# Optimization experiments

Hardware: AMD Instinct MI355X
Metric: run time of the kernel (lower is better)

## Reference

```python
import jax, jax.numpy as jnp
import numpy as np

VOCAB_BLOCK = 2048
TEMP = 1.0
EPS_LO = 0.2
EPS_HI = 0.3


def setup_inputs() -> dict:
    key = jax.random.key(0)
    k = jax.random.split(key, 6)
    B, S, D, V = 4, 1024, 2048, 32768
    hidden_states = jax.random.normal(k[0], (B, S, D), dtype=jnp.float32)
    # 0.02 init scale keeps logits O(1) so exp/logsumexp stay well-conditioned
    lm_head_kernel = jax.random.normal(k[1], (D, V), dtype=jnp.float32) * 0.02
    input_ids = jax.random.randint(k[2], (B, S), 0, V, dtype=jnp.int32)
    labels = jax.random.randint(k[3], (B, S), 0, 2, dtype=jnp.int32)
    advantages = jax.random.normal(k[4], (B,), dtype=jnp.float32)
    old_per_token_logps = jax.random.normal(k[5], (B, S - 1), dtype=jnp.float32) * 0.1
    return {
        "hidden_states": hidden_states,
        "lm_head_kernel": lm_head_kernel,
        "input_ids": input_ids,
        "labels": labels,
        "advantages": advantages,
        "old_per_token_logps": old_per_token_logps,
    }


def _fused_logps(h, kernel):
    """Streaming logsumexp over vocab blocks; never materializes [B,T,V]."""
    B, T, D = h.shape
    V = kernel.shape[1]
    nb = V // VOCAB_BLOCK
    Wb = kernel.reshape(D, nb, VOCAB_BLOCK).transpose(1, 0, 2)  # [nb, D, bs]

    def step(carry, wb):
        m, s = carry
        lg = jnp.einsum("btd,dv->btv", h, wb) / TEMP  # [B,T,bs]
        bm = lg.max(axis=-1)
        nm = jnp.maximum(m, bm)
        s = s * jnp.exp(m - nm) + jnp.exp(lg - nm[..., None]).sum(axis=-1)
        return (nm, s), None

    init = (jnp.full((B, T), -jnp.inf, dtype=h.dtype), jnp.zeros((B, T), dtype=h.dtype))
    (m, s), _ = jax.lax.scan(step, init, Wb)
    return m + jnp.log(s)  # logsumexp over full vocab, [B,T]


def reference(hidden_states, lm_head_kernel, input_ids, labels, advantages, old_per_token_logps):
    h = hidden_states[:, :-1, :]            # [B,T,D], T = S-1
    chosen = input_ids[:, 1:]               # [B,T]
    mask = labels[:, 1:].astype(jnp.float32)

    # chosen-token logit: gather kernel columns, no full logits tensor
    w_sel = lm_head_kernel.T[chosen]        # [B,T,D]
    chosen_logit = jnp.einsum("btd,btd->bt", h, w_sel) / TEMP

    lse = _fused_logps(h, lm_head_kernel)
    per_token_logps = chosen_logit - lse    # [B,T]

    ratio = jnp.exp(per_token_logps - old_per_token_logps)
    adv = advantages[:, None]
    loss1 = ratio * adv
    loss2 = jnp.clip(ratio, 1.0 - EPS_LO, 1.0 + EPS_HI) * adv
    per_token_loss = -jnp.minimum(loss1, loss2)

    total_valid = mask.sum()
    loss = (per_token_loss * mask).sum() / total_valid
    return loss, jax.lax.stop_gradient(per_token_logps)
```

## Files before the change

### kernel.cpp

```cpp
#include <hip/hip_runtime.h>
#include <hip/hip_bf16.h>

typedef unsigned short u16;
typedef unsigned char u8;
typedef unsigned long long u64;
typedef __attribute__((ext_vector_type(4))) int i32x4;
typedef __attribute__((ext_vector_type(8))) int i32x8;
typedef __attribute__((ext_vector_type(4))) float f32x4;

#define NROWS 4092
#define NROWS_PAD 4096
#define DDIM 2048
#define VDIM 32768
#define NCHUNK 512
#define SC8 0x7F7F7F7F
#define BUFB 65536u

__device__ __forceinline__ u8 f2fp8(float f) {
  union { float f; unsigned u; } v; v.f = f;
  unsigned s = (v.u >> 24) & 0x80u;
  unsigned a = v.u & 0x7FFFFFFFu;
  if (a >= 0x43E80000u) return (u8)(s | 0x7E);
  int e = (int)(a >> 23) - 127;
  unsigned m = a & 0x7FFFFFu;
  if (e < -6) {
    unsigned full = m | 0x800000u;
    int sh = 20 + (-6 - e);
    if (sh > 31) return (u8)s;
    unsigned q = full >> sh;
    unsigned rem = full & ((1u << sh) - 1u), half = 1u << (sh - 1);
    q += (rem > half || (rem == half && (q & 1u)));
    return (u8)(s | q);
  }
  unsigned q = m >> 20, rem = m & 0xFFFFFu;
  q += (rem > 0x80000u || (rem == 0x80000u && (q & 1u)));
  unsigned bits = (((unsigned)(e + 7)) << 3) + q;
  if (bits >= 0x7Fu) bits = 0x7Eu;
  return (u8)(s | bits);
}

__device__ __forceinline__ void gload16(const void* g, void* l) {
  using gp_t = const __attribute__((address_space(1))) unsigned*;
  using lp_t = __attribute__((address_space(3))) unsigned*;
  __builtin_amdgcn_global_load_lds((gp_t)g, (lp_t)(unsigned)(unsigned long long)l,
                                   16, 0, 0);
}

#define BAR() __builtin_amdgcn_s_barrier()
#define SB()  __builtin_amdgcn_sched_barrier(0)
#define SHUF(a, b) __builtin_shufflevector(a, b, 0, 1, 2, 3, 4, 5, 6, 7)

__global__ void init_k(const int* __restrict__ ids, int* __restrict__ chosen,
                       float* __restrict__ chlog, float* __restrict__ accum) {
  int i = blockIdx.x * 256 + threadIdx.x;
  if (i < NROWS_PAD) {
    int v = -1;
    if (i < NROWS) { int b = i / 1023, t = i % 1023; v = ids[b * 1024 + t + 1]; }
    chosen[i] = v;
    chlog[i] = 0.f;
  }
  if (i < 2) accum[i] = 0.f;
}

__global__ void bucket_k(const int* __restrict__ chosen,
                         int* __restrict__ boff, int* __restrict__ bent) {
  __shared__ int cnt[512];
  __shared__ int base[512];
  int tid = threadIdx.x;
  cnt[tid] = 0;
  __syncthreads();
  int loc[8], tile[8];
#pragma unroll
  for (int j = 0; j < 8; ++j) {
    int r = tid + (j << 9);
    int c = chosen[r];
    int ti = (c < 0) ? 512 : (c >> 6);
    tile[j] = ti;
    loc[j] = (ti < 512) ? atomicAdd(&cnt[ti], 1) : 0;
  }
  __syncthreads();
  if (tid == 0) {
    int s = 0;
    for (int i = 0; i < 512; ++i) { base[i] = s; s += cnt[i]; }
  }
  __syncthreads();
  boff[tid] = base[tid];
  if (tid == 511) boff[512] = base[511] + cnt[511];
#pragma unroll
  for (int j = 0; j < 8; ++j) {
    int r = tid + (j << 9);
    if (tile[j] < 512) bent[base[tile[j]] + loc[j]] = (r << 6) | (chosen[r] & 63);
  }
}

__global__ void conv_h(const float* __restrict__ hs, u8* __restrict__ h8) {
  int idx = blockIdx.x * 256 + threadIdx.x;
  int row = idx >> 8;
  int c8 = (idx & 255) << 3;
  u64 o = 0;
  if (row < NROWS) {
    int b = row / 1023, t = row % 1023;
    const float* p = hs + (size_t)((b << 10) + t) * DDIM + c8;
    float4 x = *(const float4*)p, y = *(const float4*)(p + 4);
    o = (u64)f2fp8(x.x * 16.f)        | ((u64)f2fp8(x.y * 16.f) << 8) |
        ((u64)f2fp8(x.z * 16.f) << 16) | ((u64)f2fp8(x.w * 16.f) << 24) |
        ((u64)f2fp8(y.x * 16.f) << 32) | ((u64)f2fp8(y.y * 16.f) << 40) |
        ((u64)f2fp8(y.z * 16.f) << 48) | ((u64)f2fp8(y.w * 16.f) << 56);
  }
  *(u64*)(h8 + (size_t)row * DDIM + c8) = o;
}

__global__ void transpose_w(const float* __restrict__ W, u8* __restrict__ WT8,
                            const float* __restrict__ hs,
                            const int* __restrict__ boff,
                            const int* __restrict__ bent,
                            float* __restrict__ chlog) {
  __shared__ float t32[64][65];
  __shared__ u8 t8[64][68];
  int v0 = blockIdx.x << 6, d0 = blockIdx.y << 6;
  int tid = threadIdx.x;
  int vi = (tid & 15) << 2, dl = tid >> 4;
#pragma unroll
  for (int i = 0; i < 4; ++i) {
    int d = dl + (i << 4);
    float4 w = *(const float4*)(W + (size_t)(d0 + d) * VDIM + v0 + vi);
    t32[d][vi + 0] = w.x; t32[d][vi + 1] = w.y;
    t32[d][vi + 2] = w.z; t32[d][vi + 3] = w.w;
    t8[d][vi + 0] = f2fp8(w.x * 64.f); t8[d][vi + 1] = f2fp8(w.y * 64.f);
    t8[d][vi + 2] = f2fp8(w.z * 64.f); t8[d][vi + 3] = f2fp8(w.w * 64.f);
  }
  __syncthreads();
  int vr = tid >> 2, dc = (tid & 3) << 4;
  union { u8 b[16]; ulonglong2 q; } u;
#pragma unroll
  for (int k = 0; k < 16; ++k) u.b[k] = t8[dc + k][vr];
  *(ulonglong2*)(WT8 + (size_t)(v0 + vr) * DDIM + d0 + dc) = u.q;
  int m0 = boff[blockIdx.x], m1 = boff[blockIdx.x + 1];
  int lane = tid & 63, wv = tid >> 6;
  for (int m = m0 + wv; m < m1; m += 4) {
    int e = bent[m];
    int r = e >> 6, cv = e & 63;
    int b = r / 1023, tt = r % 1023;
    float s = hs[(size_t)((b << 10) + tt) * DDIM + d0 + lane] * t32[lane][cv];
#pragma unroll
    for (int o = 1; o < 64; o <<= 1) s += __shfl_xor(s, o, 64);
    if (lane == 0) atomicAdd(chlog + r, s);
  }
}

__global__ __launch_bounds__(256, 1) void gemm_lse(
    const u8* __restrict__ A, const u8* __restrict__ Bt,
    float2* __restrict__ partials) {
  extern __shared__ u16 smem[];
  char* lds = (char*)smem;

  const int tid = threadIdx.x;
  const int l = tid & 63;
  const int wid = tid >> 6;
  const int wmr = wid >> 1, wnr = wid & 1;
  const int ln = l & 15;
  const int g4 = l >> 4;
  const int xr = ln & 7;

  int bid = blockIdx.x;
  int id = ((bid & 7) << 8) | (bid >> 3);
  int bm = id & 15;
  int bn = id >> 4;
  const int m0 = bm << 8, n0 = bn << 8;

  const u8* Ab = A + (size_t)m0 * DDIM;
  const u8* Bb = Bt + (size_t)n0 * DDIM;

  const unsigned aA0 = (unsigned)((wmr << 14) + (ln << 7)) + (((0 | g4) ^ xr) << 4);
  const unsigned aA1 = (unsigned)((wmr << 14) + (ln << 7)) + (((4 | g4) ^ xr) << 4);
  const unsigned aB0 = 32768u + (unsigned)((wnr << 14) + (ln << 7)) + (((0 | g4) ^ xr) << 4);
  const unsigned aB1 = 32768u + (unsigned)((wnr << 14) + (ln << 7)) + (((4 | g4) ^ xr) << 4);

  const int srow = l >> 3;
  const unsigned selb = (unsigned)(((l & 7) ^ srow) << 4);
  unsigned voff[8];
#pragma unroll
  for (int j = 0; j < 8; ++j)
    voff[j] = (unsigned)(((((j << 2) + wid) << 3) | srow) * 2048) + selb;

#define RFL(x) __builtin_amdgcn_readfirstlane((int)(x))
#define GLL(src, dst) gload16((src), lds + RFL(dst))
#define LD4(off) (*(const i32x4*)(lds + (off)))
#define FRAG(b0, b1, o) SHUF(LD4((b0) + (o)), LD4((b1) + (o)))
#define DSTA(j) (unsigned)((((j) << 2) + wid) << 10)
#define DSTB(j) (32768u + (unsigned)((((j) << 2) + wid) << 10))

  f32x4 acc[8][8] = {};

#pragma unroll
  for (int j = 0; j < 8; ++j) GLL(Ab + voff[j], DSTA(j));
#pragma unroll
  for (int j = 0; j < 8; ++j) GLL(Bb + voff[j], DSTB(j));
  asm volatile("s_waitcnt vmcnt(0)" ::: "memory"); SB();
  BAR();
  SB();

  for (int t = 0; t < 16; ++t) {
    const unsigned fb = (unsigned)(t & 1) * BUFB;
    const unsigned fbn = BUFB - fb;
    const u8* baseA = Ab + ((t + 1) << 7);
    const u8* baseB = Bb + ((t + 1) << 7);
    const unsigned rA0 = fb + aA0, rA1 = fb + aA1;
    const unsigned rB0 = fb + aB0, rB1 = fb + aB1;

    i32x8 bf[8];
#pragma unroll
    for (int ni = 0; ni < 8; ++ni) bf[ni] = FRAG(rB0, rB1, ni * 2048);

#pragma unroll
    for (int mi = 0; mi < 8; ++mi) {
      i32x8 af = FRAG(rA0, rA1, mi * 2048);
      if (t < 15) {
        if (mi < 4) { GLL(baseA + voff[2 * mi], fbn + DSTA(2 * mi));
                      GLL(baseA + voff[2 * mi + 1], fbn + DSTA(2 * mi + 1)); }
        else { int j = 2 * (mi - 4);
               GLL(baseB + voff[j], fbn + DSTB(j));
               GLL(baseB + voff[j + 1], fbn + DSTB(j + 1)); }
      }
      __builtin_amdgcn_s_setprio(1);
#pragma unroll
      for (int ni = 0; ni < 8; ++ni)
        acc[mi][ni] = __builtin_amdgcn_mfma_scale_f32_16x16x128_f8f6f4(
            af, bf[ni], acc[mi][ni], 0, 0, 0, SC8, 0, SC8);
      __builtin_amdgcn_s_setprio(0);
    }
    if (t < 15) { asm volatile("s_waitcnt vmcnt(0)" ::: "memory"); }
    SB();
    BAR();
    SB();
  }

  const int chunk0 = (bn << 2) | (wnr << 1);
#pragma unroll
  for (int mi = 0; mi < 8; ++mi) {
#pragma unroll
    for (int rr = 0; rr < 4; ++rr) {
      const int row = m0 + (wmr << 7) + (mi << 4) + (g4 << 2) + rr;
#pragma unroll
      for (int h = 0; h < 2; ++h) {
        float v0 = acc[mi][4 * h + 0][rr] * 0.0009765625f;
        float v1 = acc[mi][4 * h + 1][rr] * 0.0009765625f;
        float v2 = acc[mi][4 * h + 2][rr] * 0.0009765625f;
        float v3 = acc[mi][4 * h + 3][rr] * 0.0009765625f;
        float mx = fmaxf(fmaxf(v0, v1), fmaxf(v2, v3));
#pragma unroll
        for (int o = 1; o < 16; o <<= 1) mx = fmaxf(mx, __shfl_xor(mx, o, 64));
        float s = __expf(v0 - mx) + __expf(v1 - mx) + __expf(v2 - mx) + __expf(v3 - mx);
#pragma unroll
        for (int o = 1; o < 16; o <<= 1) s += __shfl_xor(s, o, 64);
        if (ln == 0) partials[(size_t)row * NCHUNK + chunk0 + h] = make_float2(mx, s);
      }
    }
  }
#undef DSTA
#undef DSTB
#undef FRAG
#undef LD4
#undef GLL
#undef RFL
}

__global__ void reduce_lse(const float2* __restrict__ partials,
                           const float* __restrict__ chlog,
                           const float* __restrict__ oldlp,
                           const int* __restrict__ labels,
                           const float* __restrict__ adv,
                           float* __restrict__ out, float* __restrict__ accum) {
  const int wid = threadIdx.x >> 6, l = threadIdx.x & 63;
  const int row = blockIdx.x * 4 + wid;
  float M = -INFINITY, S = 0.f;
  for (int c = l; c < NCHUNK; c += 64) {
    float2 p = partials[(size_t)row * NCHUNK + c];
    float Mn = fmaxf(M, p.x);
    S = S * __expf(M - Mn) + p.y * __expf(p.x - Mn);
    M = Mn;
  }
#pragma unroll
  for (int o = 1; o < 64; o <<= 1) {
    float Mo = __shfl_xor(M, o, 64), So = __shfl_xor(S, o, 64);
    float Mn = fmaxf(M, Mo);
    S = S * __expf(M - Mn) + So * __expf(Mo - Mn);
    M = Mn;
  }
  if (l == 0) {
    float lse = M + __logf(S);
    float ptl = chlog[row] - lse;
    out[1 + row] = ptl;
    int b = row / 1023, t = row % 1023;
    float a = adv[b];
    float ratio = __expf(ptl - oldlp[row]);
    float l1 = ratio * a;
    float l2 = fminf(fmaxf(ratio, 0.8f), 1.3f) * a;
    float mk = (float)labels[b * 1024 + t + 1];
    atomicAdd(accum + 0, -fminf(l1, l2) * mk);
    atomicAdd(accum + 1, mk);
  }
}

__global__ void finalize_k(const float* __restrict__ accum, float* __restrict__ out) {
  out[0] = accum[0] / accum[1];
}

extern "C" void kernel_launch(void* const* d_in, const int* in_sizes, int n_in,
                              void* d_out, int out_size, void* d_ws, size_t ws_size,
                              hipStream_t stream) {
  const float* hs     = (const float*)d_in[0];
  const float* W      = (const float*)d_in[1];
  const int*   ids    = (const int*)d_in[2];
  const int*   labels = (const int*)d_in[3];
  const float* adv    = (const float*)d_in[4];
  const float* oldlp  = (const float*)d_in[5];
  float* out = (float*)d_out;

  char* ws = (char*)d_ws;
  u8*     WT8      = (u8*)ws;
  u8*     h8       = (u8*)(ws + 67108864);
  float2* partials = (float2*)(ws + 75497472);
  float*  chlog    = (float*)(ws + 92274688);
  int*    chosen   = (int*)(ws + 92291072);
  float*  accum    = (float*)(ws + 92307456);
  int*    boff     = (int*)(ws + 92307520);
  int*    bent     = (int*)(ws + 92309632);

  (void)hipFuncSetAttribute((const void*)gemm_lse,
                            hipFuncAttributeMaxDynamicSharedMemorySize, 131072);

  init_k<<<16, 256, 0, stream>>>(ids, chosen, chlog, accum);
  bucket_k<<<1, 512, 0, stream>>>(chosen, boff, bent);
  conv_h<<<4096, 256, 0, stream>>>(hs, h8);
  transpose_w<<<dim3(512, 32), 256, 0, stream>>>(W, WT8, hs, boff, bent, chlog);
  gemm_lse<<<2048, 256, 131072, stream>>>(h8, WT8, partials);
  reduce_lse<<<1023, 256, 0, stream>>>(partials, chlog, oldlp, labels, adv, out, accum);
  finalize_k<<<1, 1, 0, stream>>>(accum, out);
}
```

Measured before the change: 600.5 us.

## Split GEMM tile across eight waves with 128x64 per-wave subtiles

Doubles the workgroup to 512 threads so eight waves share the 256x256 tile, each computing 128x64 instead of 128x128. Accumulator registers per wave halve, and more waves are available to hide latency. Global-to-LDS loads are redistributed across the eight waves, and the LSE epilogue writes one partial per wave chunk. In exchange, LDS fragment reads per MFMA increase and operand reuse per wave drops.

```diff
diff --git a/kernel.cpp b/kernel.cpp
--- a/kernel.cpp
+++ b/kernel.cpp
@@ -148,7 +148,7 @@
   }
 }
 
-__global__ __launch_bounds__(256, 1) void gemm_lse(
+__global__ __launch_bounds__(512, 2) void gemm_lse(
     const u8* __restrict__ A, const u8* __restrict__ Bt,
     float2* __restrict__ partials) {
   extern __shared__ u16 smem[];
@@ -157,7 +157,7 @@
   const int tid = threadIdx.x;
   const int l = tid & 63;
   const int wid = tid >> 6;
-  const int wmr = wid >> 1, wnr = wid & 1;
+  const int wm = wid >> 2, wn = wid & 3;
   const int ln = l & 15;
   const int g4 = l >> 4;
   const int xr = ln & 7;
@@ -171,31 +171,31 @@
   const u8* Ab = A + (size_t)m0 * DDIM;
   const u8* Bb = Bt + (size_t)n0 * DDIM;
 
-  const unsigned aA0 = (unsigned)((wmr << 14) + (ln << 7)) + (((0 | g4) ^ xr) << 4);
-  const unsigned aA1 = (unsigned)((wmr << 14) + (ln << 7)) + (((4 | g4) ^ xr) << 4);
-  const unsigned aB0 = 32768u + (unsigned)((wnr << 14) + (ln << 7)) + (((0 | g4) ^ xr) << 4);
-  const unsigned aB1 = 32768u + (unsigned)((wnr << 14) + (ln << 7)) + (((4 | g4) ^ xr) << 4);
+  const unsigned aA0 = (unsigned)((wm << 14) + (ln << 7)) + (((0 | g4) ^ xr) << 4);
+  const unsigned aA1 = (unsigned)((wm << 14) + (ln << 7)) + (((4 | g4) ^ xr) << 4);
+  const unsigned aB0 = 32768u + (unsigned)((wn << 13) + (ln << 7)) + (((0 | g4) ^ xr) << 4);
+  const unsigned aB1 = 32768u + (unsigned)((wn << 13) + (ln << 7)) + (((4 | g4) ^ xr) << 4);
 
   const int srow = l >> 3;
   const unsigned selb = (unsigned)(((l & 7) ^ srow) << 4);
-  unsigned voff[8];
-#pragma unroll
-  for (int j = 0; j < 8; ++j)
-    voff[j] = (unsigned)(((((j << 2) + wid) << 3) | srow) * 2048) + selb;
+  unsigned voff[4];
+#pragma unroll
+  for (int j = 0; j < 4; ++j)
+    voff[j] = (unsigned)(((((j << 3) + wid) << 3) | srow) * 2048) + selb;
 
 #define RFL(x) __builtin_amdgcn_readfirstlane((int)(x))
 #define GLL(src, dst) gload16((src), lds + RFL(dst))
 #define LD4(off) (*(const i32x4*)(lds + (off)))
 #define FRAG(b0, b1, o) SHUF(LD4((b0) + (o)), LD4((b1) + (o)))
-#define DSTA(j) (unsigned)((((j) << 2) + wid) << 10)
-#define DSTB(j) (32768u + (unsigned)((((j) << 2) + wid) << 10))
-
-  f32x4 acc[8][8] = {};
-
-#pragma unroll
-  for (int j = 0; j < 8; ++j) GLL(Ab + voff[j], DSTA(j));
-#pragma unroll
-  for (int j = 0; j < 8; ++j) GLL(Bb + voff[j], DSTB(j));
+#define DSTA(j) (unsigned)((((j) << 3) + wid) << 10)
+#define DSTB(j) (32768u + (unsigned)((((j) << 3) + wid) << 10))
+
+  f32x4 acc[8][4] = {};
+
+#pragma unroll
+  for (int j = 0; j < 4; ++j) GLL(Ab + voff[j], DSTA(j));
+#pragma unroll
+  for (int j = 0; j < 4; ++j) GLL(Bb + voff[j], DSTB(j));
   asm volatile("s_waitcnt vmcnt(0)" ::: "memory"); SB();
   BAR();
   SB();
@@ -208,25 +208,28 @@
     const unsigned rA0 = fb + aA0, rA1 = fb + aA1;
     const unsigned rB0 = fb + aB0, rB1 = fb + aB1;
 
-    i32x8 bf[8];
-#pragma unroll
-    for (int ni = 0; ni < 8; ++ni) bf[ni] = FRAG(rB0, rB1, ni * 2048);
-
-#pragma unroll
-    for (int mi = 0; mi < 8; ++mi) {
-      i32x8 af = FRAG(rA0, rA1, mi * 2048);
+    i32x8 af[8];
+#pragma unroll
+    for (int mi = 0; mi < 8; ++mi) af[mi] = FRAG(rA0, rA1, mi * 2048);
+
+#pragma unroll
+    for (int ni = 0; ni < 4; ++ni) {
+      i32x8 bf = FRAG(rB0, rB1, ni * 2048);
       if (t < 15) {
-        if (mi < 4) { GLL(baseA + voff[2 * mi], fbn + DSTA(2 * mi));
-                      GLL(baseA + voff[2 * mi + 1], fbn + DSTA(2 * mi + 1)); }
-        else { int j = 2 * (mi - 4);
-               GLL(baseB + voff[j], fbn + DSTB(j));
-               GLL(baseB + voff[j + 1], fbn + DSTB(j + 1)); }
+        if (ni == 0)      { GLL(baseA + voff[0], fbn + DSTA(0));
+                            GLL(baseA + voff[1], fbn + DSTA(1)); }
+        else if (ni == 1) { GLL(baseA + voff[2], fbn + DSTA(2));
+                            GLL(baseA + voff[3], fbn + DSTA(3)); }
+        else if (ni == 2) { GLL(baseB + voff[0], fbn + DSTB(0));
+                            GLL(baseB + voff[1], fbn + DSTB(1)); }
+        else              { GLL(baseB + voff[2], fbn + DSTB(2));
+                            GLL(baseB + voff[3], fbn + DSTB(3)); }
       }
       __builtin_amdgcn_s_setprio(1);
 #pragma unroll
-      for (int ni = 0; ni < 8; ++ni)
+      for (int mi = 0; mi < 8; ++mi)
         acc[mi][ni] = __builtin_amdgcn_mfma_scale_f32_16x16x128_f8f6f4(
-            af, bf[ni], acc[mi][ni], 0, 0, 0, SC8, 0, SC8);
+            af[mi], bf, acc[mi][ni], 0, 0, 0, SC8, 0, SC8);
       __builtin_amdgcn_s_setprio(0);
     }
     if (t < 15) { asm volatile("s_waitcnt vmcnt(0)" ::: "memory"); }
@@ -235,26 +238,23 @@
     SB();
   }
 
-  const int chunk0 = (bn << 2) | (wnr << 1);
+  const int chunk = (bn << 2) | wn;
 #pragma unroll
   for (int mi = 0; mi < 8; ++mi) {
 #pragma unroll
     for (int rr = 0; rr < 4; ++rr) {
-      const int row = m0 + (wmr << 7) + (mi << 4) + (g4 << 2) + rr;
-#pragma unroll
-      for (int h = 0; h < 2; ++h) {
-        float v0 = acc[mi][4 * h + 0][rr] * 0.0009765625f;
-        float v1 = acc[mi][4 * h + 1][rr] * 0.0009765625f;
-        float v2 = acc[mi][4 * h + 2][rr] * 0.0009765625f;
-        float v3 = acc[mi][4 * h + 3][rr] * 0.0009765625f;
-        float mx = fmaxf(fmaxf(v0, v1), fmaxf(v2, v3));
-#pragma unroll
-        for (int o = 1; o < 16; o <<= 1) mx = fmaxf(mx, __shfl_xor(mx, o, 64));
-        float s = __expf(v0 - mx) + __expf(v1 - mx) + __expf(v2 - mx) + __expf(v3 - mx);
-#pragma unroll
-        for (int o = 1; o < 16; o <<= 1) s += __shfl_xor(s, o, 64);
-        if (ln == 0) partials[(size_t)row * NCHUNK + chunk0 + h] = make_float2(mx, s);
-      }
+      const int row = m0 + (wm << 7) + (mi << 4) + (g4 << 2) + rr;
+      float v0 = acc[mi][0][rr] * 0.0009765625f;
+      float v1 = acc[mi][1][rr] * 0.0009765625f;
+      float v2 = acc[mi][2][rr] * 0.0009765625f;
+      float v3 = acc[mi][3][rr] * 0.0009765625f;
+      float mx = fmaxf(fmaxf(v0, v1), fmaxf(v2, v3));
+#pragma unroll
+      for (int o = 1; o < 16; o <<= 1) mx = fmaxf(mx, __shfl_xor(mx, o, 64));
+      float s = __expf(v0 - mx) + __expf(v1 - mx) + __expf(v2 - mx) + __expf(v3 - mx);
+#pragma unroll
+      for (int o = 1; o < 16; o <<= 1) s += __shfl_xor(s, o, 64);
+      if (ln == 0) partials[(size_t)row * NCHUNK + chunk] = make_float2(mx, s);
     }
   }
 #undef DSTA
@@ -334,7 +334,7 @@
   bucket_k<<<1, 512, 0, stream>>>(chosen, boff, bent);
   conv_h<<<4096, 256, 0, stream>>>(hs, h8);
   transpose_w<<<dim3(512, 32), 256, 0, stream>>>(W, WT8, hs, boff, bent, chlog);
-  gemm_lse<<<2048, 256, 131072, stream>>>(h8, WT8, partials);
+  gemm_lse<<<2048, 512, 131072, stream>>>(h8, WT8, partials);
   reduce_lse<<<1023, 256, 0, stream>>>(partials, chlog, oldlp, labels, adv, out, accum);
   finalize_k<<<1, 1, 0, stream>>>(accum, out);
 }
```

Result: faster. 508.2 us (-15.4%).
